# Optimization experiments

Measured on AMD Instinct MI355X. Metric: run time of the kernel, lower is better.

## Reference

```python
import jax, jax.numpy as jnp
import numpy as np
from jax import lax

B, D, H, W = 2, 96, 96, 96
K = 3          # static upper bound on connected components (setup builds exactly 3 blobs)
CC_ITERS = 48  # >= max component diameter under 26-connectivity label propagation
V = D * H * W
BIGI = jnp.int32(V)  # sentinel label for background


def _make_target():
    # 3 well-separated spherical lesions per volume -> exactly K connected components
    centers = [(20, 20, 20), (70, 30, 60), (40, 75, 75)]
    r2 = 9 ** 2
    zz, yy, xx = np.meshgrid(np.arange(D), np.arange(H), np.arange(W), indexing='ij')
    vol = np.zeros((D, H, W), np.float32)
    for cz, cy, cx in centers:
        vol[(zz - cz) ** 2 + (yy - cy) ** 2 + (xx - cx) ** 2 <= r2] = 1.0
    return jnp.asarray(np.stack([vol, np.roll(vol, 5, axis=2)])[:, None])  # [B,1,D,H,W]


def setup_inputs() -> dict:
    key = jax.random.key(0)
    pred = jax.random.normal(key, (B, 1, D, H, W), jnp.float32)
    return {"pred": pred, "target": _make_target()}


def _connected_components(mask):
    # 26-connectivity labeling (matches skimage/cucim default for 3D).
    # Label = min flat raster index in each component, so ascending-sorted labels
    # reproduce cucim's scan-order labels 1..N (needed for tie-breaking parity).
    lab = jnp.where(mask, jnp.arange(V, dtype=jnp.int32).reshape(mask.shape), BIGI)
    for _ in range(CC_ITERS):  # fixed unroll; components have diameter << CC_ITERS
        nb = lax.reduce_window(lab, BIGI, lax.min, (3, 3, 3), (1, 1, 1), 'SAME')
        lab = jnp.where(mask, nb, BIGI)
    return lab


def _edt1d(f):
    # exact 1D squared-distance lower envelope: d[i] = min_j f[j] + (i-j)^2
    n = f.shape[-1]
    i = jnp.arange(n, dtype=jnp.float32)
    sq = (i[:, None] - i[None, :]) ** 2  # [n_out, n_in]
    return jnp.min(f[..., None, :] + sq, axis=-1)


def _squared_edt(seed):
    # exact squared Euclidean distance-to-seed via 3 separable passes
    f = jnp.where(seed, jnp.float32(0), jnp.float32(1e12))
    for ax in range(3):
        f = jnp.moveaxis(_edt1d(jnp.moveaxis(f, ax, -1)), -1, ax)
    return f


def _forward(pred, target):
    p = jax.nn.sigmoid(pred)[:, 0]  # dim==5 -> sigmoid; squeeze channel -> [B,D,H,W]
    g = target[:, 0]

    def labels(gt):
        lab = _connected_components(gt > 0.5)
        ul = jnp.unique(lab, size=K + 1, fill_value=BIGI)[:K]  # ascending = scan order
        return lab, ul

    lab, ul = jax.vmap(labels)(g)                 # lab [B,D,H,W], ul [B,K]
    valid = (ul < BIGI).astype(p.dtype)           # [B,K]
    seeds = lab[:, None] == ul[:, :, None, None, None]  # [B,K,D,H,W] bool
    # serial map over (B*K) regions keeps the [D,H,W,n] EDT intermediate to one at a time
    dists = lax.map(_squared_edt, seeds.reshape(B * K, D, H, W)).reshape(B, K, D, H, W)
    # squared vs sqrt distance: same ordering AND same ties as torch's strict '<' update;
    rmap = jnp.argmin(dists, axis=1)              # Voronoi region map [B,D,H,W]

    oh = jax.nn.one_hot(rmap, K, dtype=p.dtype)   # [B,D,H,W,K]
    inter = jnp.einsum('bdhw,bdhwk->bk', p * g, oh)
    psum = jnp.einsum('bdhw,bdhwk->bk', p, oh)
    gsum = jnp.einsum('bdhw,bdhwk->bk', g, oh)
    dice = 2.0 * inter / (psum + gsum + 1e-8)
    cnt = jnp.sum(valid, axis=1)
    mean_dice = jnp.sum(dice * valid, axis=1) / jnp.maximum(cnt, 1.0)
    loss = jnp.where(cnt > 0, 1.0 - mean_dice, 1.0)  # num_features==0 -> loss 1.0
    return jnp.mean(loss)


def reference(pred, target):
    return _forward(pred, target)
```

## Files before the change

kernel.cpp:

```cpp
#include <hip/hip_runtime.h>
#include <math.h>

#define SLICE 9216
#define VOL 884736
#define NB 2
#define KK 3
#define BIGI VOL
#define BIGP 0x3FFFFFFC
#define BIGPF 1.0e9f
#define CC_SWEEPS 3
#define NYC 4
#define NZC 4
#define NPART (NB*96*NZC)
#define MAXROW 64
#define MAXNZ 64
#define YSTR (MAXNZ*96)

#define OFF_ACT   (NB*VOL*4)
#define OFF_DISTC (2*NB*VOL*4)
#define DISTC_BYTES (NB*96*MAXNZ*96*4)
#define OFF_SMALL (OFF_DISTC + DISTC_BYTES)
#define OFF_ZMASK (OFF_SMALL + 64)
#define OFF_ROOTS (OFF_SMALL + 128)
#define OFF_REL   (OFF_SMALL + 1024)
#define OFF_ARR   (OFF_SMALL + 3072)
#define OFF_FCNT  (OFF_SMALL + 6144)
#define OFF_MASK  (OFF_SMALL + 8192)
#define MASK_ULL  (NB*KK*96*96*2)
#define OFF_PART  (OFF_MASK + MASK_ULL*8)

__device__ __forceinline__ int ldA_i(const int* p) {
  return __hip_atomic_load(p, __ATOMIC_RELAXED, __HIP_MEMORY_SCOPE_AGENT);
}
__device__ __forceinline__ unsigned long long ldA_u64(const unsigned long long* p) {
  return __hip_atomic_load(p, __ATOMIC_RELAXED, __HIP_MEMORY_SCOPE_AGENT);
}
__device__ __forceinline__ float ldA_f(const float* p) {
  return __hip_atomic_load(p, __ATOMIC_RELAXED, __HIP_MEMORY_SCOPE_AGENT);
}
__device__ __forceinline__ void stA_i(int* p, int v) {
  __hip_atomic_store(p, v, __ATOMIC_RELAXED, __HIP_MEMORY_SCOPE_AGENT);
}
__device__ __forceinline__ void stA_u64(unsigned long long* p, unsigned long long v) {
  __hip_atomic_store(p, v, __ATOMIC_RELAXED, __HIP_MEMORY_SCOPE_AGENT);
}
__device__ __forceinline__ void stA_f(float* p, float v) {
  __hip_atomic_store(p, v, __ATOMIC_RELAXED, __HIP_MEMORY_SCOPE_AGENT);
}

__device__ __forceinline__ void gbar(int* arr, int* rel, int ph) {
  __syncthreads();
  asm volatile("" ::: "memory");
  if (blockIdx.x == 0) {
    const int t = threadIdx.x;
    if (t) { while (ldA_i(&arr[t]) <= ph) __builtin_amdgcn_s_sleep(2); }
    while (ldA_i(&arr[t + 256]) <= ph) __builtin_amdgcn_s_sleep(2);
    while (ldA_i(&arr[t + 512]) <= ph) __builtin_amdgcn_s_sleep(2);
    __syncthreads();
    if (t < 16) stA_i(&rel[t << 5], ph + 1);
  } else {
    if (threadIdx.x == 0) {
      stA_i(&arr[blockIdx.x], ph + 1);
      while (ldA_i(&rel[(blockIdx.x & 15) << 5]) <= ph)
        __builtin_amdgcn_s_sleep(4);
    }
  }
  asm volatile("" ::: "memory");
  __syncthreads();
}

struct EdtSh {
  unsigned long long sM[KK * 192];
  float pl[MAXROW * 96];
  unsigned char vrow[96];
  int s_n;
};
struct FuseSh {
  float g[MAXNZ * 96];
  unsigned char zl[96];
  int s_last;
  float wsum[4][9];
  float fs[4][18];
};
struct SeedSh {
  int s_roots[128];
  int s_ul[NB][KK];
  unsigned long long zm[NB * 2];
};
union MegaSh { EdtSh edt; FuseSh fuse; SeedSh seed; };

__device__ __forceinline__ int row_dist(unsigned long long lo,
                                        unsigned long long hi, int x) {
  int dr, dlft;
  {
    unsigned long long rl, rh;
    if (x == 0)      { rl = lo; rh = hi; }
    else if (x < 64) { rl = (lo >> x) | (hi << (64 - x)); rh = hi >> x; }
    else             { rl = hi >> (x - 64); rh = 0; }
    dr = rl ? (__ffsll(rl) - 1) : (rh ? (63 + __ffsll(rh)) : 1000);
  }
  {
    unsigned long long ll, lh;
    if (x >= 64) { ll = lo; lh = hi & ((2ull << (x - 64)) - 1); }
    else         { ll = lo & ((2ull << x) - 1); lh = 0; }
    dlft = lh ? (x - 127 + __clzll(lh))
              : (ll ? (x - 63 + __clzll(ll)) : 1000);
  }
  return min(dr, dlft);
}

__global__ __launch_bounds__(256, 3) void k_mega(
    const float* __restrict__ pred, const float* __restrict__ tgt,
    int* __restrict__ lab, int* __restrict__ act, float* __restrict__ distC,
    int* __restrict__ small, unsigned long long* __restrict__ zmg,
    int* __restrict__ roots, unsigned long long* __restrict__ masks,
    float* __restrict__ part, int* __restrict__ arr, int* __restrict__ rel,
    int* __restrict__ fcnt, float* __restrict__ out) {
  __shared__ MegaSh sh;
  const int t = threadIdx.x;
  const int lane = t & 63;
  const int gid = blockIdx.x * 256 + t;
  const int gstr = gridDim.x * 256;

  {
    const float4* tgt4 = (const float4*)tgt;
    for (int q = gid; q < MASK_ULL; q += gstr) stA_u64(&masks[q], 0ull);
    for (int q = gid; q < NB * VOL / 4; q += gstr) {
      float4 tv = tgt4[q];
      int base = q * 4;
      int bo = (base >= VOL) ? VOL : 0;
      int4 lv;
      lv.x = (tv.x > 0.5f) ? base - bo     : BIGI;
      lv.y = (tv.y > 0.5f) ? base - bo + 1 : BIGI;
      lv.z = (tv.z > 0.5f) ? base - bo + 2 : BIGI;
      lv.w = (tv.w > 0.5f) ? base - bo + 3 : BIGI;
      unsigned long long w0 = (unsigned)lv.x | ((unsigned long long)(unsigned)lv.y << 32);
      unsigned long long w1 = (unsigned)lv.z | ((unsigned long long)(unsigned)lv.w << 32);
      stA_u64((unsigned long long*)lab + 2 * q,     w0);
      stA_u64((unsigned long long*)lab + 2 * q + 1, w1);
      int cnt = (lv.x != BIGI) + (lv.y != BIGI) + (lv.z != BIGI) + (lv.w != BIGI);
      int pre = cnt;
      #pragma unroll
      for (int off = 1; off < 64; off <<= 1) {
        int v = __shfl_up(pre, off, 64);
        if (lane >= off) pre += v;
      }
      int total = __shfl(pre, 63, 64);
      if (total) {
        int base_ws = 0;
        if (lane == 63) base_ws = atomicAdd(&small[0], total);
        base_ws = __shfl(base_ws, 63, 64);
        int pos = base_ws + pre - cnt;
        if (lv.x != BIGI) stA_i(&act[pos++], base);
        if (lv.y != BIGI) stA_i(&act[pos++], base + 1);
        if (lv.z != BIGI) stA_i(&act[pos++], base + 2);
        if (lv.w != BIGI) stA_i(&act[pos],   base + 3);
      }
    }
  }
  gbar(arr, rel, 0);

  for (int sweep = 0; sweep < CC_SWEEPS; sweep++) {
    const int record = (sweep == CC_SWEEPS - 1) ? 1 : 0;
    const int n = ldA_i(&small[0]);
    for (int i = gid; i < n; i += gstr) {
      int idx = ldA_i(&act[i]);
      int bo = (idx >= VOL) ? VOL : 0;
      int v = idx - bo;
      int z = v / SLICE;
      int rem = v - z * SLICE;
      int y = rem / 96;
      int x = rem - y * 96;
      int* L = lab + bo;
      int z0 = z > 0 ? z - 1 : 0, z1 = z < 95 ? z + 1 : 95;
      int y0 = y > 0 ? y - 1 : 0, y1 = y < 95 ? y + 1 : 95;
      int x0 = x > 0 ? x - 1 : 0, x1 = x < 95 ? x + 1 : 95;
      int m = BIGI;
      for (int zz = z0; zz <= z1; zz++)
        for (int yy = y0; yy <= y1; yy++) {
          const int* row = L + zz * SLICE + yy * 96;
          for (int xx = x0; xx <= x1; xx++) m = min(m, ldA_i(&row[xx]));
        }
      int m2 = ldA_i(&L[m]);
      int m3 = ldA_i(&L[m2]);
      int m4 = ldA_i(&L[m3]);
      stA_i(&lab[idx], m4);
      if (record && m4 == v) {
        int b = bo ? 1 : 0;
        int pos = atomicAdd(&small[1 + b], 1);
        if (pos < 64) stA_i(&roots[b * 64 + pos], v);
      }
    }
    gbar(arr, rel, 1 + sweep);
  }

  {
    if (t < 128) {
      int b = t >> 6, j = t & 63;
      int nr = ldA_i(&small[1 + b]); if (nr > 64) nr = 64;
      sh.seed.s_roots[t] = (j < nr) ? ldA_i(&roots[t]) : 0x7fffffff;
    }
    if (t < NB * KK) sh.seed.s_ul[t / KK][t % KK] = -2;
    if (t < NB * 2) sh.seed.zm[t] = 0;
    __syncthreads();
    if (t < 128) {
      int r = sh.seed.s_roots[t];
      if (r != 0x7fffffff) {
        int b = t >> 6;
        int rank = 0;
        #pragma unroll
        for (int j = 0; j < 64; j++)
          rank += (sh.seed.s_roots[(b << 6) + j] < r) ? 1 : 0;
        if (rank < KK) sh.seed.s_ul[b][rank] = r;
      }
    }
    __syncthreads();
    const int n = ldA_i(&small[0]);
    for (int i = gid; i < n; i += gstr) {
      int idx = ldA_i(&act[i]);
      int b = (idx >= VOL) ? 1 : 0;
      int v = idx - (b ? VOL : 0);
      int lv = ldA_i(&lab[idx]);
      int k = (lv == sh.seed.s_ul[b][0]) ? 0 : (lv == sh.seed.s_ul[b][1]) ? 1
            : (lv == sh.seed.s_ul[b][2]) ? 2 : -1;
      if (k >= 0) {
        int z = v / SLICE;
        int rem = v - z * SLICE;
        int y = rem / 96;
        int x = rem - y * 96;
        unsigned long long* M =
            masks + (((size_t)(b * KK + k) * 96 + z) * 96 + y) * 2;
        if (x < 64) atomicOr(&M[0], 1ull << x);
        else        atomicOr(&M[1], 1ull << (x - 64));
        if (z < 64) atomicOr(&sh.seed.zm[b * 2],     1ull << z);
        else        atomicOr(&sh.seed.zm[b * 2 + 1], 1ull << (z - 64));
      }
    }
    __syncthreads();
    if (t < NB * 2 && sh.seed.zm[t]) atomicOr(&zmg[t], sh.seed.zm[t]);
  }
  gbar(arr, rel, 4);

  {
    int blk = blockIdx.x;
    if (blk < NB * MAXNZ * NYC) {
      int b = blk / (MAXNZ * NYC);
      int rem = blk - b * MAXNZ * NYC;
      int jj = rem / NYC;
      int yc = rem - jj * NYC;
      unsigned long long zlo = ldA_u64(&zmg[b * 2]);
      unsigned long long zhi = ldA_u64(&zmg[b * 2 + 1]);
      int nlo = __popcll(zlo);
      int nz = nlo + __popcll(zhi);
      if (jj < nz) {
        int z;
        if (jj < nlo) {
          unsigned long long w = zlo;
          for (int i = 0; i < jj; i++) w &= w - 1;
          z = __ffsll(w) - 1;
        } else {
          unsigned long long w = zhi;
          int r2 = jj - nlo;
          for (int i = 0; i < r2; i++) w &= w - 1;
          z = 64 + __ffsll(w) - 1;
        }
        if (t == 0) sh.edt.s_n = 0;
        for (int i = t; i < KK * 192; i += 256) {
          int k = i / 192, r = i - k * 192;
          sh.edt.sM[i] = ldA_u64(&masks[((size_t)(b * KK + k) * 96 + z) * 192 + r]);
        }
        __syncthreads();
        if (t < 96) {
          unsigned long long any = sh.edt.sM[t * 2] | sh.edt.sM[t * 2 + 1] |
                                   sh.edt.sM[192 + t * 2] | sh.edt.sM[193 + t * 2] |
                                   sh.edt.sM[384 + t * 2] | sh.edt.sM[385 + t * 2];
          if (any) {
            int pos = atomicAdd(&sh.edt.s_n, 1);
            if (pos < MAXROW) sh.edt.vrow[pos] = (unsigned char)t;
          }
        }
        __syncthreads();
        int n = sh.edt.s_n; if (n > MAXROW) n = MAXROW;
        for (int i = t; i < n * 96; i += 256) {
          int j2 = i / 96, x = i - j2 * 96;
          int y = sh.edt.vrow[j2];
          int best = BIGP;
          #pragma unroll
          for (int k = 0; k < KK; k++) {
            unsigned long long lo = sh.edt.sM[k * 192 + y * 2];
            unsigned long long hi = sh.edt.sM[k * 192 + y * 2 + 1];
            if (lo | hi) {
              int d = row_dist(lo, hi, x);
              best = min(best, ((d * d) << 2) | k);
            }
          }
          sh.edt.pl[j2 * 96 + x] = (best == BIGP) ? BIGPF : (float)best;
        }
        __syncthreads();
        for (int tt = t; tt < 288; tt += 256) {
          int x = tt % 96;
          int yg = tt / 96;
          int yy0 = yc * 24 + yg * 8;
          float acc[8];
          #pragma unroll
          for (int i2 = 0; i2 < 8; i2++) acc[i2] = BIGPF;
          for (int j2 = 0; j2 < n; j2++) {
            int j = sh.edt.vrow[j2];
            float f = sh.edt.pl[j2 * 96 + x];
            float d0 = (float)(yy0 - j);
            #pragma unroll
            for (int i2 = 0; i2 < 8; i2++) {
              float dy = d0 + (float)i2;
              acc[i2] = fminf(acc[i2], __builtin_fmaf(4.f * dy, dy, f));
            }
          }
          float* DA = distC + (size_t)b * 96 * YSTR + jj * 96 + x;
          #pragma unroll
          for (int i2 = 0; i2 < 8; i2++)
            stA_f(&DA[(yy0 + i2) * YSTR], acc[i2]);
        }
      }
    }
  }
  gbar(arr, rel, 5);

  {
    int blk = blockIdx.x;
    int b = blk / (96 * NZC);
    int rem = blk - b * 96 * NZC;
    int y = rem / NZC;
    int zc = rem - y * NZC;
    unsigned long long zlo = ldA_u64(&zmg[b * 2]);
    unsigned long long zhi = ldA_u64(&zmg[b * 2 + 1]);
    int nz = __popcll(zlo) + __popcll(zhi);
    if (nz > MAXNZ) nz = MAXNZ;
    if (t < 96) {
      int set = (t < 64) ? (int)((zlo >> t) & 1) : (int)((zhi >> (t - 64)) & 1);
      if (set) {
        int jj;
        if (t < 64) jj = __popcll(zlo & ((t ? (1ull << t) : 1ull) - 1ull));
        else        jj = __popcll(zlo) + __popcll(zhi & ((1ull << (t - 64)) - 1ull));
        if (jj < MAXNZ) sh.fuse.zl[jj] = (unsigned char)t;
      }
    }
    {
      const unsigned long long* src8 =
          (const unsigned long long*)(distC + (size_t)(b * 96 + y) * YSTR);
      unsigned long long* g8 = (unsigned long long*)sh.fuse.g;
      int n8 = nz * 48;
      for (int i = t; i < n8; i += 256) g8[i] = ldA_u64(src8 + i);
    }
    __syncthreads();
    const float* P = pred + (size_t)b * VOL + y * 96;
    const float* G = tgt + (size_t)b * VOL + y * 96;
    float a0 = 0.f, a1 = 0.f, a2 = 0.f, a3 = 0.f, a4 = 0.f,
          a5 = 0.f, a6 = 0.f, a7 = 0.f, a8 = 0.f;
    for (int tt = t; tt < 288; tt += 256) {
      int x = tt % 96;
      int zg = tt / 96;
      int zz0 = zc * 24 + zg * 8;
      float pv[8], gv[8];
      #pragma unroll
      for (int i2 = 0; i2 < 8; i2++) {
        int off = (zz0 + i2) * SLICE + x;
        pv[i2] = P[off];
        gv[i2] = G[off];
      }
      float acc[8];
      #pragma unroll
      for (int i2 = 0; i2 < 8; i2++) acc[i2] = BIGPF;
      for (int jj = 0; jj < nz; jj++) {
        float f = sh.fuse.g[jj * 96 + x];
        float d0 = (float)(zz0 - (int)sh.fuse.zl[jj]);
        #pragma unroll
        for (int i2 = 0; i2 < 8; i2++) {
          float dz = d0 + (float)i2;
          acc[i2] = fminf(acc[i2], __builtin_fmaf(4.f * dz, dz, f));
        }
      }
      #pragma unroll
      for (int i2 = 0; i2 < 8; i2++) {
        float p = __builtin_amdgcn_rcpf(1.f + __expf(-pv[i2]));
        float gg = gv[i2];
        int kk = ((int)acc[i2]) & 3;
        float pg = p * gg;
        a0 += (kk == 0) ? pg : 0.f;
        a1 += (kk == 1) ? pg : 0.f;
        a2 += (kk == 2) ? pg : 0.f;
        a3 += (kk == 0) ? p : 0.f;
        a4 += (kk == 1) ? p : 0.f;
        a5 += (kk == 2) ? p : 0.f;
        a6 += (kk == 0) ? gg : 0.f;
        a7 += (kk == 1) ? gg : 0.f;
        a8 += (kk == 2) ? gg : 0.f;
      }
    }
    float s[9] = {a0, a1, a2, a3, a4, a5, a6, a7, a8};
    #pragma unroll
    for (int off = 32; off > 0; off >>= 1)
      #pragma unroll
      for (int q = 0; q < 9; q++) s[q] += __shfl_down(s[q], off);
    int wave = t >> 6, lane2 = t & 63;
    if (lane2 == 0) {
      #pragma unroll
      for (int q = 0; q < 9; q++) sh.fuse.wsum[wave][q] = s[q];
    }
    __syncthreads();
    if (t < 9)
      stA_f(&part[blk * 9 + t], sh.fuse.wsum[0][t] + sh.fuse.wsum[1][t] +
                                sh.fuse.wsum[2][t] + sh.fuse.wsum[3][t]);
    __syncthreads();
    if (t == 0) {
      sh.fuse.s_last = 0;
      int f = atomicAdd(&fcnt[(blk & 15) << 5], 1);
      if (f == NPART / 16 - 1) {
        int w = atomicAdd(&small[3], 1);
        sh.fuse.s_last = (w == 15) ? 1 : 0;
      }
    }
    __syncthreads();
    if (!sh.fuse.s_last) return;
    float a[18];
    #pragma unroll
    for (int q = 0; q < 18; q++) a[q] = 0.f;
    for (int r = t; r < NPART; r += 256) {
      int bb = r / (96 * NZC);
      #pragma unroll
      for (int q = 0; q < 9; q++) a[bb * 9 + q] += ldA_f(&part[r * 9 + q]);
    }
    #pragma unroll
    for (int off = 32; off > 0; off >>= 1)
      #pragma unroll
      for (int q = 0; q < 18; q++) a[q] += __shfl_down(a[q], off);
    if (lane2 == 0) {
      #pragma unroll
      for (int q = 0; q < 18; q++) sh.fuse.fs[wave][q] = a[q];
    }
    __syncthreads();
    if (t == 0) {
      float tot[18];
      #pragma unroll
      for (int q = 0; q < 18; q++)
        tot[q] = sh.fuse.fs[0][q] + sh.fuse.fs[1][q] +
                 sh.fuse.fs[2][q] + sh.fuse.fs[3][q];
      float loss = 0.f;
      for (int bb = 0; bb < NB; bb++) {
        int cnt = ldA_i(&small[1 + bb]);
        if (cnt > KK) cnt = KK;
        float ds = 0.f;
        for (int k = 0; k < cnt; k++) {
          float inter = tot[bb * 9 + k];
          float ps = tot[bb * 9 + 3 + k];
          float gs = tot[bb * 9 + 6 + k];
          ds += 2.f * inter / (ps + gs + 1e-8f);
        }
        float mean = ds / fmaxf((float)cnt, 1.f);
        loss += (cnt > 0) ? (1.f - mean) : 1.f;
      }
      out[0] = loss * 0.5f;
    }
  }
}

extern "C" void kernel_launch(void* const* d_in, const int* in_sizes, int n_in,
                              void* d_out, int out_size, void* d_ws, size_t ws_size,
                              hipStream_t stream) {
  const float* pred = (const float*)d_in[0];
  const float* tgt  = (const float*)d_in[1];
  float* out = (float*)d_out;

  char* ws = (char*)d_ws;
  int* lab   = (int*)(ws);
  int* act   = (int*)(ws + OFF_ACT);
  float* distC = (float*)(ws + OFF_DISTC);
  int* small = (int*)(ws + OFF_SMALL);
  unsigned long long* zmg = (unsigned long long*)(ws + OFF_ZMASK);
  int* roots = (int*)(ws + OFF_ROOTS);
  int* rel   = (int*)(ws + OFF_REL);
  int* arrv  = (int*)(ws + OFF_ARR);
  int* fcnt  = (int*)(ws + OFF_FCNT);
  unsigned long long* masks = (unsigned long long*)(ws + OFF_MASK);
  float* part = (float*)(ws + OFF_PART);

  hipMemsetAsync(ws + OFF_SMALL, 0, 8192, stream);

  void* args[] = { (void*)&pred, (void*)&tgt, (void*)&lab, (void*)&act,
                   (void*)&distC, (void*)&small, (void*)&zmg, (void*)&roots,
                   (void*)&masks, (void*)&part, (void*)&arrv, (void*)&rel,
                   (void*)&fcnt, (void*)&out };
  hipLaunchCooperativeKernel((void*)k_mega, dim3(NPART), dim3(256), args, 0,
                             stream);
}
```

Baseline: 161.9 us.

## Fold first CC sweep into init and build seed masks per-slice in EDT stage

The init pass now computes each foreground voxel's initial label as the minimum foreground index in its 3x3x3 neighbourhood, which stands in for one propagation sweep, so only two sweeps remain. The separate seed-mask stage, with its global bitmask array, its zeroing and one grid barrier, is removed. Each EDT block instead ranks the roots and builds its z-slice masks in shared memory directly from the label array. This trades two grid barriers and the global atomics for redundant per-block root ranking and a full slice scan of labels, plus 27 target reads per foreground voxel at init.

```diff
diff --git a/kernel.cpp b/kernel.cpp
--- a/kernel.cpp
+++ b/kernel.cpp
@@ -8,7 +8,6 @@
 #define BIGI VOL
 #define BIGP 0x3FFFFFFC
 #define BIGPF 1.0e9f
-#define CC_SWEEPS 3
 #define NYC 4
 #define NZC 4
 #define NPART (NB*96*NZC)
@@ -25,9 +24,7 @@
 #define OFF_REL   (OFF_SMALL + 1024)
 #define OFF_ARR   (OFF_SMALL + 3072)
 #define OFF_FCNT  (OFF_SMALL + 6144)
-#define OFF_MASK  (OFF_SMALL + 8192)
-#define MASK_ULL  (NB*KK*96*96*2)
-#define OFF_PART  (OFF_MASK + MASK_ULL*8)
+#define OFF_PART  (OFF_SMALL + 8192)
 
 __device__ __forceinline__ int ldA_i(const int* p) {
   return __hip_atomic_load(p, __ATOMIC_RELAXED, __HIP_MEMORY_SCOPE_AGENT);
@@ -74,6 +71,8 @@
   float pl[MAXROW * 96];
   unsigned char vrow[96];
   int s_n;
+  int s_roots[64];
+  int s_ul[KK];
 };
 struct FuseSh {
   float g[MAXNZ * 96];
@@ -82,12 +81,7 @@
   float wsum[4][9];
   float fs[4][18];
 };
-struct SeedSh {
-  int s_roots[128];
-  int s_ul[NB][KK];
-  unsigned long long zm[NB * 2];
-};
-union MegaSh { EdtSh edt; FuseSh fuse; SeedSh seed; };
+union MegaSh { EdtSh edt; FuseSh fuse; };
 
 __device__ __forceinline__ int row_dist(unsigned long long lo,
                                         unsigned long long hi, int x) {
@@ -113,10 +107,10 @@
     const float* __restrict__ pred, const float* __restrict__ tgt,
     int* __restrict__ lab, int* __restrict__ act, float* __restrict__ distC,
     int* __restrict__ small, unsigned long long* __restrict__ zmg,
-    int* __restrict__ roots, unsigned long long* __restrict__ masks,
-    float* __restrict__ part, int* __restrict__ arr, int* __restrict__ rel,
-    int* __restrict__ fcnt, float* __restrict__ out) {
+    int* __restrict__ roots, float* __restrict__ part, int* __restrict__ arr,
+    int* __restrict__ rel, int* __restrict__ fcnt, float* __restrict__ out) {
   __shared__ MegaSh sh;
+  __shared__ unsigned long long s_zm[4];
   const int t = threadIdx.x;
   const int lane = t & 63;
   const int gid = blockIdx.x * 256 + t;
@@ -124,26 +118,52 @@
 
   {
     const float4* tgt4 = (const float4*)tgt;
-    for (int q = gid; q < MASK_ULL; q += gstr) stA_u64(&masks[q], 0ull);
+    if (t < 4) s_zm[t] = 0;
+    __syncthreads();
     for (int q = gid; q < NB * VOL / 4; q += gstr) {
       float4 tv = tgt4[q];
       int base = q * 4;
       int bo = (base >= VOL) ? VOL : 0;
-      int4 lv;
-      lv.x = (tv.x > 0.5f) ? base - bo     : BIGI;
-      lv.y = (tv.y > 0.5f) ? base - bo + 1 : BIGI;
-      lv.z = (tv.z > 0.5f) ? base - bo + 2 : BIGI;
-      lv.w = (tv.w > 0.5f) ? base - bo + 3 : BIGI;
-      unsigned long long w0 = (unsigned)lv.x | ((unsigned long long)(unsigned)lv.y << 32);
-      unsigned long long w1 = (unsigned)lv.z | ((unsigned long long)(unsigned)lv.w << 32);
+      int v0 = base - bo;
+      int z = v0 / SLICE;
+      int rem0 = v0 - z * SLICE;
+      int y = rem0 / 96;
+      int x0 = rem0 - y * 96;
+      const float* T = tgt + bo;
+      float tvs[4] = {tv.x, tv.y, tv.z, tv.w};
+      int lv[4];
+      int cnt = 0;
+      int z0 = z > 0 ? z - 1 : 0, z1 = z < 95 ? z + 1 : 95;
+      int y0 = y > 0 ? y - 1 : 0, y1 = y < 95 ? y + 1 : 95;
+      #pragma unroll
+      for (int j = 0; j < 4; j++) {
+        if (tvs[j] > 0.5f) {
+          int x = x0 + j;
+          int xa = x > 0 ? x - 1 : 0, xb = x < 95 ? x + 1 : 95;
+          int m = BIGI;
+          for (int zz = z0; zz <= z1; zz++)
+            for (int yy = y0; yy <= y1; yy++) {
+              const float* row = T + zz * SLICE + yy * 96;
+              for (int xx = xa; xx <= xb; xx++)
+                if (row[xx] > 0.5f) m = min(m, zz * SLICE + yy * 96 + xx);
+            }
+          lv[j] = m;
+          cnt++;
+        } else lv[j] = BIGI;
+      }
+      unsigned long long w0 = (unsigned)lv[0] | ((unsigned long long)(unsigned)lv[1] << 32);
+      unsigned long long w1 = (unsigned)lv[2] | ((unsigned long long)(unsigned)lv[3] << 32);
       stA_u64((unsigned long long*)lab + 2 * q,     w0);
       stA_u64((unsigned long long*)lab + 2 * q + 1, w1);
-      int cnt = (lv.x != BIGI) + (lv.y != BIGI) + (lv.z != BIGI) + (lv.w != BIGI);
+      if (cnt) {
+        int bb = bo ? 1 : 0;
+        atomicOr(&s_zm[bb * 2 + (z >= 64)], 1ull << (z & 63));
+      }
       int pre = cnt;
       #pragma unroll
       for (int off = 1; off < 64; off <<= 1) {
-        int v = __shfl_up(pre, off, 64);
-        if (lane >= off) pre += v;
+        int vv = __shfl_up(pre, off, 64);
+        if (lane >= off) pre += vv;
       }
       int total = __shfl(pre, 63, 64);
       if (total) {
@@ -151,17 +171,19 @@
         if (lane == 63) base_ws = atomicAdd(&small[0], total);
         base_ws = __shfl(base_ws, 63, 64);
         int pos = base_ws + pre - cnt;
-        if (lv.x != BIGI) stA_i(&act[pos++], base);
-        if (lv.y != BIGI) stA_i(&act[pos++], base + 1);
-        if (lv.z != BIGI) stA_i(&act[pos++], base + 2);
-        if (lv.w != BIGI) stA_i(&act[pos],   base + 3);
-      }
-    }
+        if (lv[0] != BIGI) stA_i(&act[pos++], base);
+        if (lv[1] != BIGI) stA_i(&act[pos++], base + 1);
+        if (lv[2] != BIGI) stA_i(&act[pos++], base + 2);
+        if (lv[3] != BIGI) stA_i(&act[pos],   base + 3);
+      }
+    }
+    __syncthreads();
+    if (t < 4 && s_zm[t]) atomicOr(&zmg[t], s_zm[t]);
   }
   gbar(arr, rel, 0);
 
-  for (int sweep = 0; sweep < CC_SWEEPS; sweep++) {
-    const int record = (sweep == CC_SWEEPS - 1) ? 1 : 0;
+  for (int sweep = 0; sweep < 2; sweep++) {
+    const int record = sweep;
     const int n = ldA_i(&small[0]);
     for (int i = gid; i < n; i += gstr) {
       int idx = ldA_i(&act[i]);
@@ -193,53 +215,6 @@
     }
     gbar(arr, rel, 1 + sweep);
   }
-
-  {
-    if (t < 128) {
-      int b = t >> 6, j = t & 63;
-      int nr = ldA_i(&small[1 + b]); if (nr > 64) nr = 64;
-      sh.seed.s_roots[t] = (j < nr) ? ldA_i(&roots[t]) : 0x7fffffff;
-    }
-    if (t < NB * KK) sh.seed.s_ul[t / KK][t % KK] = -2;
-    if (t < NB * 2) sh.seed.zm[t] = 0;
-    __syncthreads();
-    if (t < 128) {
-      int r = sh.seed.s_roots[t];
-      if (r != 0x7fffffff) {
-        int b = t >> 6;
-        int rank = 0;
-        #pragma unroll
-        for (int j = 0; j < 64; j++)
-          rank += (sh.seed.s_roots[(b << 6) + j] < r) ? 1 : 0;
-        if (rank < KK) sh.seed.s_ul[b][rank] = r;
-      }
-    }
-    __syncthreads();
-    const int n = ldA_i(&small[0]);
-    for (int i = gid; i < n; i += gstr) {
-      int idx = ldA_i(&act[i]);
-      int b = (idx >= VOL) ? 1 : 0;
-      int v = idx - (b ? VOL : 0);
-      int lv = ldA_i(&lab[idx]);
-      int k = (lv == sh.seed.s_ul[b][0]) ? 0 : (lv == sh.seed.s_ul[b][1]) ? 1
-            : (lv == sh.seed.s_ul[b][2]) ? 2 : -1;
-      if (k >= 0) {
-        int z = v / SLICE;
-        int rem = v - z * SLICE;
-        int y = rem / 96;
-        int x = rem - y * 96;
-        unsigned long long* M =
-            masks + (((size_t)(b * KK + k) * 96 + z) * 96 + y) * 2;
-        if (x < 64) atomicOr(&M[0], 1ull << x);
-        else        atomicOr(&M[1], 1ull << (x - 64));
-        if (z < 64) atomicOr(&sh.seed.zm[b * 2],     1ull << z);
-        else        atomicOr(&sh.seed.zm[b * 2 + 1], 1ull << (z - 64));
-      }
-    }
-    __syncthreads();
-    if (t < NB * 2 && sh.seed.zm[t]) atomicOr(&zmg[t], sh.seed.zm[t]);
-  }
-  gbar(arr, rel, 4);
 
   {
     int blk = blockIdx.x;
@@ -264,10 +239,37 @@
           for (int i = 0; i < r2; i++) w &= w - 1;
           z = 64 + __ffsll(w) - 1;
         }
+        if (t < 64) {
+          int nr = ldA_i(&small[1 + b]); if (nr > 64) nr = 64;
+          sh.edt.s_roots[t] = (t < nr) ? ldA_i(&roots[b * 64 + t]) : 0x7fffffff;
+        }
+        if (t < KK) sh.edt.s_ul[t] = -2;
         if (t == 0) sh.edt.s_n = 0;
-        for (int i = t; i < KK * 192; i += 256) {
-          int k = i / 192, r = i - k * 192;
-          sh.edt.sM[i] = ldA_u64(&masks[((size_t)(b * KK + k) * 96 + z) * 192 + r]);
+        for (int i = t; i < KK * 192; i += 256) sh.edt.sM[i] = 0;
+        __syncthreads();
+        if (t < 64) {
+          int r = sh.edt.s_roots[t];
+          if (r != 0x7fffffff) {
+            int rank = 0;
+            #pragma unroll
+            for (int j = 0; j < 64; j++)
+              rank += (sh.edt.s_roots[j] < r) ? 1 : 0;
+            if (rank < KK) sh.edt.s_ul[rank] = r;
+          }
+        }
+        __syncthreads();
+        const int* Lb = lab + b * VOL + z * SLICE;
+        int u0 = sh.edt.s_ul[0], u1 = sh.edt.s_ul[1], u2 = sh.edt.s_ul[2];
+        for (int i = t; i < SLICE; i += 256) {
+          int lvv = ldA_i(&Lb[i]);
+          if (lvv != BIGI) {
+            int k = (lvv == u0) ? 0 : (lvv == u1) ? 1 : (lvv == u2) ? 2 : -1;
+            if (k >= 0) {
+              int yy = i / 96, xx = i - yy * 96;
+              atomicOr(&sh.edt.sM[k * 192 + yy * 2 + (xx >> 6)],
+                       1ull << (xx & 63));
+            }
+          }
         }
         __syncthreads();
         if (t < 96) {
@@ -322,7 +324,7 @@
       }
     }
   }
-  gbar(arr, rel, 5);
+  gbar(arr, rel, 3);
 
   {
     int blk = blockIdx.x;
@@ -479,15 +481,14 @@
   int* rel   = (int*)(ws + OFF_REL);
   int* arrv  = (int*)(ws + OFF_ARR);
   int* fcnt  = (int*)(ws + OFF_FCNT);
-  unsigned long long* masks = (unsigned long long*)(ws + OFF_MASK);
   float* part = (float*)(ws + OFF_PART);
 
   hipMemsetAsync(ws + OFF_SMALL, 0, 8192, stream);
 
   void* args[] = { (void*)&pred, (void*)&tgt, (void*)&lab, (void*)&act,
                    (void*)&distC, (void*)&small, (void*)&zmg, (void*)&roots,
-                   (void*)&masks, (void*)&part, (void*)&arrv, (void*)&rel,
-                   (void*)&fcnt, (void*)&out };
+                   (void*)&part, (void*)&arrv, (void*)&rel, (void*)&fcnt,
+                   (void*)&out };
   hipLaunchCooperativeKernel((void*)k_mega, dim3(NPART), dim3(256), args, 0,
                              stream);
 }
```

Result: slower. 197.0 us (+21.7%).
